# Kernel tuning notes

Measured on AMD Instinct MI355X. Metric: run time of the kernel, lower is better.

The kernel has to match this reference:

```python
import jax, jax.numpy as jnp
import numpy as np
import math

B, T, D = 1, 2048, 2048
H, HD = 16, 128          # n_head, head_dim = D // H
L = 512                  # latent_dims
RD = 64                  # rope_dims
K = 32                   # top-k selected tokens per query
THETA = 10000.0


def rope_tables(rd, t_max):
    freqs = 1.0 / (THETA ** (jnp.arange(0, rd, 2, dtype=jnp.float32) / rd))
    t = jnp.arange(t_max, dtype=jnp.float32)
    ang = jnp.outer(t, freqs)                      # (T, rd/2)
    cos = jnp.concatenate([jnp.cos(ang), jnp.cos(ang)], axis=-1)  # (T, rd)
    sin = jnp.concatenate([jnp.sin(ang), jnp.sin(ang)], axis=-1)
    return cos, sin


def rotate_half(x):
    d = x.shape[-1] // 2
    return jnp.concatenate([-x[..., d:], x[..., :d]], axis=-1)


def apply_rope(x, cos, sin):
    # x: (B, H, T, rd); cos/sin: (T, rd) -> broadcast over B, H
    t = x.shape[2]
    return x * cos[None, None, :t] + rotate_half(x) * sin[None, None, :t]


def setup_inputs() -> dict:
    key = jax.random.key(0)
    ks = jax.random.split(key, 10)
    s = lambda fan_in: 1.0 / math.sqrt(fan_in)
    inp = {
        'x': jax.random.normal(ks[0], (B, T, D), dtype=jnp.float32),
        'Wqd': jax.random.normal(ks[1], (D, L), dtype=jnp.float32) * s(D),
        'Wqu': jax.random.normal(ks[2], (L, D), dtype=jnp.float32) * s(L),
        'Wqr': jax.random.normal(ks[3], (L, H * RD), dtype=jnp.float32) * s(L),
        'Wkvd': jax.random.normal(ks[4], (D, L), dtype=jnp.float32) * s(D),
        'Wku': jax.random.normal(ks[5], (L, D), dtype=jnp.float32) * s(L),
        'Wvu': jax.random.normal(ks[6], (L, D), dtype=jnp.float32) * s(L),
        'Wkr': jax.random.normal(ks[7], (D, RD), dtype=jnp.float32) * s(D),
        'Wo': jax.random.normal(ks[8], (D, D), dtype=jnp.float32) * s(D),
        'topk_idx': jax.random.randint(ks[9], (B, T, K), 0, T, dtype=jnp.int64)
            if jax.config.jax_enable_x64 else
            jax.random.randint(ks[9], (B, T, K), 0, T, dtype=jnp.int32),
    }
    return inp


def reference(x, Wqd, Wqu, Wqr, Wkvd, Wku, Wvu, Wkr, Wo, topk_idx):
    cos, sin = rope_tables(RD, T)

    ql = x @ Wqd                                               # (B,T,L)
    q = (ql @ Wqu).reshape(B, T, H, HD).transpose(0, 2, 1, 3)  # (B,H,T,hd)
    qr = (ql @ Wqr).reshape(B, T, H, RD).transpose(0, 2, 1, 3)
    qr = apply_rope(qr, cos, sin)                              # (B,H,T,rd)

    ckv = x @ Wkvd                                             # (B,T,L)
    k = (ckv @ Wku).reshape(B, T, H, HD).transpose(0, 2, 1, 3) # (B,H,T,hd)
    v = (ckv @ Wvu).reshape(B, T, H, HD).transpose(0, 2, 1, 3)
    kr = apply_rope((x @ Wkr)[:, None], cos, sin)[:, 0]        # (B,T,rd) shared across heads

    # top-k gather sparse attention path
    flat = topk_idx.reshape(B, T * K)                          # (B, T*K)
    k_sel = jax.vmap(lambda a, i: a[:, i])(k, flat).reshape(B, H, T, K, HD)
    v_sel = jax.vmap(lambda a, i: a[:, i])(v, flat).reshape(B, H, T, K, HD)
    kr_sel = jax.vmap(lambda a, i: a[i])(kr, flat).reshape(B, T, K, RD)

    scale = 1.0 / math.sqrt(HD + RD)
    scores = (jnp.einsum('bhtd,bhtkd->bhtk', q, k_sel)
              + jnp.einsum('bhtd,btkd->bhtk', qr, kr_sel)) * scale
    attn = jax.nn.softmax(scores, axis=-1)                     # (B,H,T,K)
    out = jnp.einsum('bhtk,bhtkd->bhtd', attn, v_sel)          # (B,H,T,hd)
    out = out.transpose(0, 2, 1, 3).reshape(B, T, D)
    return out @ Wo
```

## Files before the change

### kernel.cpp

```cpp
#include <hip/hip_runtime.h>
#include <hip/hip_bf16.h>
#include <math.h>

typedef __hip_bfloat16 bf16;
typedef __attribute__((ext_vector_type(4))) float f32x4;
typedef __attribute__((ext_vector_type(8))) short s16x8;

#define T_SEQ 2048
#define DIM   2048
#define NH    16
#define LAT   512
#define RD    64
#define TOPK  32

typedef const __attribute__((address_space(1))) void* gas_ptr;
typedef __attribute__((address_space(3))) void* las_ptr;

struct GGroup {
    const bf16* A; const bf16* BT; bf16* C;
    int K, lda, ldb, ldc;
    int tx, ty, nz;
    long aZ, bZ, cZ;
    int tiles;
    int flags, N, t0;
};
struct GPack { GGroup g[4]; int n; };

template<int MT>
__global__ __launch_bounds__(256)
void gemm_group64(GPack gp)
{
    constexpr int MI = MT / 64;
    int b = blockIdx.x;
    int gi = 0;
    while (gi < gp.n - 1 && b >= gp.g[gi].tiles) { b -= gp.g[gi].tiles; ++gi; }
    const GGroup g = gp.g[gi];

    const int per_z = g.tx * g.ty;
    const int z   = b / per_z;
    const int rem = b - z * per_z;
    const int bx  = rem % g.tx;
    const int by  = rem / g.tx;

    const bf16* A  = g.A  + (size_t)z * g.aZ;
    const bf16* BT = g.BT + (size_t)z * g.bZ;
    bf16*       C  = g.C  + (size_t)z * g.cZ;

    __shared__ bf16 aL[MT * 64];
    __shared__ bf16 bL[64 * 64];

    const int tid  = threadIdx.x;
    const int wave = tid >> 6;
    const int lane = tid & 63;
    const int quad = lane >> 4;
    const int l16  = lane & 15;

    const int tile_m = by * MT;
    const int tile_n = bx * 64;
    const int wrow = wave * (MT / 4);

    const int lrow = lane >> 3;
    const int lke  = (((lane & 7) ^ lrow) * 8);
    const int sw   = l16 & 7;

    f32x4 acc[MI][4] = {};

    for (int k0 = 0; k0 < g.K; k0 += 64) {
#pragma unroll
        for (int p = 0; p < 2 * MI; ++p) {
            const int R = (wave * 2 * MI + p) * 8;
            const bf16* src = A + (size_t)(tile_m + R + lrow) * g.lda + k0 + lke;
            __builtin_amdgcn_global_load_lds((gas_ptr)src, (las_ptr)(aL + R * 64), 16, 0, 0);
        }
#pragma unroll
        for (int p = 0; p < 2; ++p) {
            const int R = (wave * 2 + p) * 8;
            const bf16* src = BT + (size_t)(tile_n + R + lrow) * g.ldb + k0 + lke;
            __builtin_amdgcn_global_load_lds((gas_ptr)src, (las_ptr)(bL + R * 64), 16, 0, 0);
        }
        __syncthreads();

#pragma unroll
        for (int ks = 0; ks < 2; ++ks) {
            s16x8 af[MI], bfr[4];
#pragma unroll
            for (int i = 0; i < MI; ++i)
                af[i] = *(const s16x8*)(&aL[(wrow + i * 16 + l16) * 64 +
                                            (((ks * 4 + quad) ^ sw) * 8)]);
#pragma unroll
            for (int j = 0; j < 4; ++j)
                bfr[j] = *(const s16x8*)(&bL[(j * 16 + l16) * 64 +
                                             (((ks * 4 + quad) ^ sw) * 8)]);

#pragma unroll
            for (int i = 0; i < MI; ++i)
#pragma unroll
                for (int j = 0; j < 4; ++j)
                    acc[i][j] = __builtin_amdgcn_mfma_f32_16x16x32_bf16(
                        af[i], bfr[j], acc[i][j], 0, 0, 0);
        }
        __syncthreads();
    }

    if (g.flags & 1) {
#pragma unroll
        for (int jp = 0; jp < 2; ++jp) {
            const int colL = tile_n + jp * 16 + l16;
            if ((g.flags & 2) && colL >= g.N) continue;
            const float fr = powf(10000.f, -(float)(jp * 16 + l16) / 32.f);
#pragma unroll
            for (int i = 0; i < MI; ++i) {
#pragma unroll
                for (int r = 0; r < 4; ++r) {
                    const int row = tile_m + wrow + i * 16 + quad * 4 + r;
                    float sv, cv;
                    sincosf((float)(g.t0 + row) * fr, &sv, &cv);
                    const float x0 = acc[i][jp][r];
                    const float x1 = acc[i][jp + 2][r];
                    C[(size_t)row * g.ldc + colL]      = __float2bfloat16(x0 * cv - x1 * sv);
                    C[(size_t)row * g.ldc + colL + 32] = __float2bfloat16(x1 * cv + x0 * sv);
                }
            }
        }
    } else if (g.flags & 4) {
        float* Cf = (float*)C;
#pragma unroll
        for (int j = 0; j < 4; ++j) {
            const int col = tile_n + j * 16 + l16;
#pragma unroll
            for (int i = 0; i < MI; ++i)
#pragma unroll
                for (int r = 0; r < 4; ++r) {
                    const int row = tile_m + wrow + i * 16 + quad * 4 + r;
                    Cf[(size_t)row * g.ldc + col] = acc[i][j][r];
                }
        }
    } else {
#pragma unroll
        for (int j = 0; j < 4; ++j) {
            const int col = tile_n + j * 16 + l16;
            if ((g.flags & 2) && col >= g.N) continue;
#pragma unroll
            for (int i = 0; i < MI; ++i)
#pragma unroll
                for (int r = 0; r < 4; ++r) {
                    const int row = tile_m + wrow + i * 16 + quad * 4 + r;
                    C[(size_t)row * g.ldc + col] = __float2bfloat16(acc[i][j][r]);
                }
        }
    }
}

struct TDesc { const float* src; bf16* dst; int R; int C; int tiles; int ctiles; };
struct TPack { TDesc d[8]; int n; };

__global__ __launch_bounds__(256)
void transpose_batch(TPack p)
{
    int b = blockIdx.x;
    int mi = 0;
    while (mi < p.n - 1 && b >= p.d[mi].tiles) { b -= p.d[mi].tiles; ++mi; }
    const TDesc d = p.d[mi];
    const int tr = b / d.ctiles, tc = b % d.ctiles;
    const int r0 = tr * 32, c0 = tc * 32;

    __shared__ float lds[32][33];
    const int tx = threadIdx.x & 31, ty = threadIdx.x >> 5;
#pragma unroll
    for (int i = 0; i < 4; ++i)
        lds[ty * 4 + i][tx] = d.src[(size_t)(r0 + ty * 4 + i) * d.C + c0 + tx];
    __syncthreads();
#pragma unroll
    for (int i = 0; i < 4; ++i)
        d.dst[(size_t)(c0 + ty * 4 + i) * d.R + r0 + tx] =
            __float2bfloat16(lds[tx][ty * 4 + i]);
}

__global__ __launch_bounds__(256)
void convert2(const float* s0, bf16* d0, int n0,
              const float* s1, bf16* d1, int n1)
{
    int i = blockIdx.x * blockDim.x + threadIdx.x;
    const float* s; bf16* d;
    if (i < n0) { s = s0; d = d0; }
    else if (i < n0 + n1) { i -= n0; s = s1; d = d1; }
    else return;
    const float4 a = *(const float4*)(s + (size_t)i * 8);
    const float4 b = *(const float4*)(s + (size_t)i * 8 + 4);
    bf16 t[8];
    t[0] = __float2bfloat16(a.x); t[1] = __float2bfloat16(a.y);
    t[2] = __float2bfloat16(a.z); t[3] = __float2bfloat16(a.w);
    t[4] = __float2bfloat16(b.x); t[5] = __float2bfloat16(b.y);
    t[6] = __float2bfloat16(b.z); t[7] = __float2bfloat16(b.w);
    *(uint4*)(d + (size_t)i * 8) = *(uint4*)t;
}

__global__ __launch_bounds__(256)
void attn_mla(const bf16* __restrict__ qt,
              const bf16* __restrict__ qr,
              const bf16* __restrict__ xw,
              const bf16* __restrict__ kr,
              const int*  __restrict__ topk,
              bf16* __restrict__ U,
              int t0)
{
    __shared__ short ckv_s[32 * 520];
    __shared__ short qt_s[16 * 520];
    __shared__ short kr_s[32 * 72];
    __shared__ short qr_s[16 * 72];
    __shared__ short P_s[4][16 * 40];
    __shared__ int   idx_s[32];

    const int tl   = blockIdx.x;
    const int tg   = t0 + tl;
    const int tid  = threadIdx.x;
    const int wv   = tid >> 6;
    const int lane = tid & 63;
    const int quad = lane >> 4;
    const int l16  = lane & 15;

    if (tid < 32) {
        int j = topk[(size_t)tg * TOPK + tid];
        idx_s[tid] = (j < 0 || j >= T_SEQ) ? 0 : j;
    }
    __syncthreads();

#pragma unroll
    for (int i = 0; i < 8; ++i) {
        const int row = wv * 8 + i;
        const int j = idx_s[row];
        __builtin_amdgcn_global_load_lds(
            (gas_ptr)(xw + (size_t)j * 1024 + 512 + lane * 8),
            (las_ptr)(ckv_s + row * 520), 16, 0, 0);
    }
#pragma unroll
    for (int i = 0; i < 4; ++i) {
        const int seg = wv * 4 + i;
        __builtin_amdgcn_global_load_lds(
            (gas_ptr)(qt + (size_t)tl * 8192 + seg * 512 + lane * 8),
            (las_ptr)(qt_s + seg * 520), 16, 0, 0);
    }
    {
        const int row = tid >> 3, seg = tid & 7;
        const int j = idx_s[row];
        *(uint4*)(kr_s + row * 72 + seg * 8) =
            *(const uint4*)(kr + (size_t)j * RD + seg * 8);
    }
    if (tid < 128) {
        const int head = tid >> 3, seg = tid & 7;
        *(uint4*)(qr_s + head * 72 + seg * 8) =
            *(const uint4*)(qr + (size_t)tl * 1024 + head * 64 + seg * 8);
    }
    __syncthreads();

    f32x4 sc[2] = {};
#pragma unroll
    for (int ks = 0; ks < 16; ++ks) {
        s16x8 a  = *(const s16x8*)(qt_s + l16 * 520 + ks * 32 + quad * 8);
        s16x8 b0 = *(const s16x8*)(ckv_s + l16 * 520 + ks * 32 + quad * 8);
        s16x8 b1 = *(const s16x8*)(ckv_s + (16 + l16) * 520 + ks * 32 + quad * 8);
        sc[0] = __builtin_amdgcn_mfma_f32_16x16x32_bf16(a, b0, sc[0], 0, 0, 0);
        sc[1] = __builtin_amdgcn_mfma_f32_16x16x32_bf16(a, b1, sc[1], 0, 0, 0);
    }
#pragma unroll
    for (int ks = 0; ks < 2; ++ks) {
        s16x8 a  = *(const s16x8*)(qr_s + l16 * 72 + ks * 32 + quad * 8);
        s16x8 b0 = *(const s16x8*)(kr_s + l16 * 72 + ks * 32 + quad * 8);
        s16x8 b1 = *(const s16x8*)(kr_s + (16 + l16) * 72 + ks * 32 + quad * 8);
        sc[0] = __builtin_amdgcn_mfma_f32_16x16x32_bf16(a, b0, sc[0], 0, 0, 0);
        sc[1] = __builtin_amdgcn_mfma_f32_16x16x32_bf16(a, b1, sc[1], 0, 0, 0);
    }

    const float scale = 0.0721687836487032f;
    float inv[4];
    short* pw = P_s[wv];
#pragma unroll
    for (int r = 0; r < 4; ++r) {
        float s0 = sc[0][r] * scale, s1 = sc[1][r] * scale;
        float mx = fmaxf(s0, s1);
#pragma unroll
        for (int off = 1; off < 16; off <<= 1) mx = fmaxf(mx, __shfl_xor(mx, off));
        float p0 = __expf(s0 - mx), p1 = __expf(s1 - mx);
        float l = p0 + p1;
#pragma unroll
        for (int off = 1; off < 16; off <<= 1) l += __shfl_xor(l, off);
        inv[r] = 1.f / l;
        pw[(quad * 4 + r) * 40 + l16]      = __builtin_bit_cast(short, __float2bfloat16(p0));
        pw[(quad * 4 + r) * 40 + 16 + l16] = __builtin_bit_cast(short, __float2bfloat16(p1));
    }

    s16x8 ap = *(const s16x8*)(pw + l16 * 40 + quad * 8);
#pragma unroll
    for (int tt = 0; tt < 8; ++tt) {
        const int n0 = wv * 128 + tt * 16;
        s16x8 b;
#pragma unroll
        for (int j = 0; j < 8; ++j)
            b[j] = ckv_s[(quad * 8 + j) * 520 + n0 + l16];
        f32x4 u = {};
        u = __builtin_amdgcn_mfma_f32_16x16x32_bf16(ap, b, u, 0, 0, 0);
#pragma unroll
        for (int r = 0; r < 4; ++r)
            U[(size_t)tl * 8192 + (quad * 4 + r) * 512 + n0 + l16] =
                __float2bfloat16(u[r] * inv[r]);
    }
}

extern "C" void kernel_launch(void* const* d_in, const int* in_sizes, int n_in,
                              void* d_out, int out_size, void* d_ws, size_t ws_size,
                              hipStream_t stream)
{
    const float* x    = (const float*)d_in[0];
    const float* Wqd  = (const float*)d_in[1];
    const float* Wqu  = (const float*)d_in[2];
    const float* Wqr  = (const float*)d_in[3];
    const float* Wkvd = (const float*)d_in[4];
    const float* Wku  = (const float*)d_in[5];
    const float* Wvu  = (const float*)d_in[6];
    const float* Wkr  = (const float*)d_in[7];
    const float* Wo   = (const float*)d_in[8];
    const int*   topk = (const int*)d_in[9];
    float* out = (float*)d_out;

    const size_t KB = 1024;
    char* ws = (char*)d_ws;
    const bool flat = ws_size >= (size_t)128000 * KB;
    const int  TCH  = flat ? 2048 : 512;
    const int  NCH  = T_SEQ / TCH;

    size_t oXB, oWxT, oWkrT, oWquT, oWkub, oWqrT, oWvuT, oQ, oXW, oKR,
           oQR, oO, oWoT, oQT, oU;
    if (flat) {
        oXB = 0;       oWxT = 8192;   oWkrT = 12288; oWquT = 12544;
        oWkub = 14592; oWqrT = 16640; oWvuT = 17664; oQ = 19712;
        oXW = 27904;   oKR = 32000;   oQR = 32256;   oO = 36352;
        oWoT = 44544;  oQT = 52736;   oU = 85504;
    } else {
        oXW = 0;       oKR = 4096;    oWquT = 4352;  oWkub = 6400;
        oWqrT = 8448;  oWvuT = 9472;  oO = 11520;    oXB = 19712;
        oWxT = 27904;  oWkrT = 32000; oQ = 19712;    oQT = 21760;
        oQR = 29952;   oU = 30976;    oWoT = 21760;
    }
    bf16* xb   = (bf16*)(ws + oXB * KB);
    bf16* WxT  = (bf16*)(ws + oWxT * KB);
    bf16* WkrT = (bf16*)(ws + oWkrT * KB);
    bf16* WquT = (bf16*)(ws + oWquT * KB);
    bf16* Wkub = (bf16*)(ws + oWkub * KB);
    bf16* WqrT = (bf16*)(ws + oWqrT * KB);
    bf16* WvuT = (bf16*)(ws + oWvuT * KB);
    bf16* qB   = (bf16*)(ws + oQ * KB);
    bf16* xw   = (bf16*)(ws + oXW * KB);
    bf16* kr   = (bf16*)(ws + oKR * KB);
    bf16* qrC  = (bf16*)(ws + oQR * KB);
    bf16* o    = (bf16*)(ws + oO * KB);
    bf16* WoT  = (bf16*)(ws + oWoT * KB);
    bf16* qtC  = (bf16*)(ws + oQT * KB);
    bf16* uC   = (bf16*)(ws + oU * KB);

    dim3 blk(256);

    {
        int n0 = T_SEQ * DIM / 8, n1 = LAT * DIM / 8;
        convert2<<<(n0 + n1 + 255) / 256, blk, 0, stream>>>(x, xb, n0, Wku, Wkub, n1);
        TPack p;
        p.d[0] = { Wqd,  WxT,                   DIM, LAT,  (DIM/32)*(LAT/32),  LAT/32 };
        p.d[1] = { Wkvd, WxT + (size_t)LAT*DIM, DIM, LAT,  (DIM/32)*(LAT/32),  LAT/32 };
        p.d[2] = { Wkr,  WkrT,                  DIM, RD,   (DIM/32)*(RD/32),   RD/32  };
        p.d[3] = { Wqr,  WqrT,                  LAT, 1024, (LAT/32)*(1024/32), 1024/32 };
        p.d[4] = { Wvu,  WvuT,                  LAT, DIM,  (LAT/32)*(DIM/32),  DIM/32 };
        p.d[5] = { Wqu,  WquT,                  LAT, DIM,  (LAT/32)*(DIM/32),  DIM/32 };
        p.n = 6;
        int tot = 0;
        for (int i = 0; i < p.n; ++i) tot += p.d[i].tiles;
        if (flat) {
            p.d[6] = { Wo, WoT, DIM, DIM, (DIM/32)*(DIM/32), DIM/32 };
            p.n = 7; tot += p.d[6].tiles;
        }
        transpose_batch<<<tot, blk, 0, stream>>>(p);
    }

    {
        GPack gp;
        gp.g[0] = { xb, WxT,  xw, DIM, DIM, DIM, 1024, 1024/64, T_SEQ/64, 1,
                    0, 0, 0, (1024/64)*(T_SEQ/64), 0, 1024, 0 };
        gp.g[1] = { xb, WkrT, kr, DIM, DIM, DIM, RD,   1,       T_SEQ/64, 1,
                    0, 0, 0, T_SEQ/64, 1 , RD, 0 };
        gp.n = 2;
        gemm_group64<64><<<gp.g[0].tiles + gp.g[1].tiles, blk, 0, stream>>>(gp);
    }

    for (int c = 0; c < NCH; ++c) {
        const int t0 = c * TCH;
        bf16* q  = flat ? qB  + (size_t)t0 * 2048 : qB;
        bf16* qt = flat ? qtC + (size_t)t0 * 8192 : qtC;
        bf16* qr = flat ? qrC + (size_t)t0 * 1024 : qrC;
        bf16* U  = flat ? uC  + (size_t)t0 * 8192 : uC;
        const bf16* xwc = xw + (size_t)t0 * 1024;

        {
            GPack gp;
            gp.g[0] = { xwc, WquT, q,  LAT, 1024, LAT, 2048, 2048/64, TCH/128, 1,
                        0, 0, 0, (2048/64)*(TCH/128), 0, 2048, 0 };
            gp.g[1] = { xwc, WqrT, qr, LAT, 1024, LAT, 1024, 1024/64, TCH/128, 1,
                        0, 0, 0, (1024/64)*(TCH/128), 1 , 1024, t0 };
            gp.n = 2;
            gemm_group64<128><<<gp.g[0].tiles + gp.g[1].tiles, blk, 0, stream>>>(gp);
        }
        {
            GPack gp;
            gp.g[0] = { q, Wkub, qt, 128, 2048, 2048, 8192, 512/64, TCH/128, NH,
                        128, 128, 512, (512/64)*(TCH/128)*NH, 0, 512, 0 };
            gp.n = 1;
            gemm_group64<128><<<gp.g[0].tiles, blk, 0, stream>>>(gp);
        }
        attn_mla<<<TCH, blk, 0, stream>>>(qt, qr, xw, kr, topk, U, t0);
        {
            GPack gp;
            gp.g[0] = { U, WvuT, o + (size_t)t0 * DIM, LAT, 8192, LAT, DIM,
                        2, TCH/128, NH, 512, (long)128*LAT, 128,
                        2*(TCH/128)*NH, 0, 128, 0 };
            gp.n = 1;
            gemm_group64<128><<<gp.g[0].tiles, blk, 0, stream>>>(gp);
        }
    }

    if (!flat) {
        TPack p;
        p.d[0] = { Wo, WoT, DIM, DIM, (DIM/32)*(DIM/32), DIM/32 };
        p.n = 1;
        transpose_batch<<<p.d[0].tiles, blk, 0, stream>>>(p);
    }
    {
        GPack gp;
        gp.g[0] = { o, WoT, (bf16*)out, DIM, DIM, DIM, DIM,
                    DIM/64, T_SEQ/128, 1, 0, 0, 0,
                    (DIM/64)*(T_SEQ/128), 4 , DIM, 0 };
        gp.n = 1;
        gemm_group64<128><<<gp.g[0].tiles, blk, 0, stream>>>(gp);
    }
}
```

Before: 248.4 us.

## Triple-buffer GEMM LDS tiles with async global-to-LDS prefetch pipeline

Converts the grouped GEMM main loop from a single LDS buffer with load-sync-compute-sync into a three-stage ring. Tiles are prefetched two iterations ahead via global_load_lds, and explicit vmcnt waits plus raw s_barrier replace __syncthreads. The goal is to hide global memory latency behind MFMA compute. In exchange it triples LDS use, which may lower occupancy, and relies on exact vmcnt accounting being correct.

```diff
diff --git a/kernel.cpp b/kernel.cpp
--- a/kernel.cpp
+++ b/kernel.cpp
@@ -28,9 +28,11 @@
 
 template<int MT>
 __global__ __launch_bounds__(256)
-void gemm_group64(GPack gp)
+void gemm_group(GPack gp)
 {
     constexpr int MI = MT / 64;
+    constexpr int L  = 2 * MI + 2;
+
     int b = blockIdx.x;
     int gi = 0;
     while (gi < gp.n - 1 && b >= gp.g[gi].tiles) { b -= gp.g[gi].tiles; ++gi; }
@@ -46,8 +48,8 @@
     const bf16* BT = g.BT + (size_t)z * g.bZ;
     bf16*       C  = g.C  + (size_t)z * g.cZ;
 
-    __shared__ bf16 aL[MT * 64];
-    __shared__ bf16 bL[64 * 64];
+    __shared__ bf16 aL[3][MT * 64];
+    __shared__ bf16 bL[3][64 * 64];
 
     const int tid  = threadIdx.x;
     const int wave = tid >> 6;
@@ -61,36 +63,56 @@
 
     const int lrow = lane >> 3;
     const int lke  = (((lane & 7) ^ lrow) * 8);
-    const int sw   = l16 & 7;
+    const int sw   = l16 & 15 & 7;
 
     f32x4 acc[MI][4] = {};
 
-    for (int k0 = 0; k0 < g.K; k0 += 64) {
+    const int nt = g.K >> 6;
+
+    auto stage = [&](int t, int sb) {
+        const int k0 = t << 6;
 #pragma unroll
         for (int p = 0; p < 2 * MI; ++p) {
             const int R = (wave * 2 * MI + p) * 8;
             const bf16* src = A + (size_t)(tile_m + R + lrow) * g.lda + k0 + lke;
-            __builtin_amdgcn_global_load_lds((gas_ptr)src, (las_ptr)(aL + R * 64), 16, 0, 0);
+            __builtin_amdgcn_global_load_lds((gas_ptr)src, (las_ptr)(aL[sb] + R * 64), 16, 0, 0);
         }
 #pragma unroll
         for (int p = 0; p < 2; ++p) {
             const int R = (wave * 2 + p) * 8;
             const bf16* src = BT + (size_t)(tile_n + R + lrow) * g.ldb + k0 + lke;
-            __builtin_amdgcn_global_load_lds((gas_ptr)src, (las_ptr)(bL + R * 64), 16, 0, 0);
-        }
-        __syncthreads();
+            __builtin_amdgcn_global_load_lds((gas_ptr)src, (las_ptr)(bL[sb] + R * 64), 16, 0, 0);
+        }
+    };
+
+    stage(0, 0);
+    if (nt > 1) stage(1, 1);
+
+    int s = 0;
+    for (int t = 0; t < nt; ++t) {
+        if (t + 2 < nt) {
+            int sn = s + 2; if (sn >= 3) sn -= 3;
+            stage(t + 2, sn);
+            asm volatile("s_waitcnt vmcnt(%0)" :: "n"(2 * L) : "memory");
+        } else if (t + 1 < nt) {
+            asm volatile("s_waitcnt vmcnt(%0)" :: "n"(L) : "memory");
+        } else {
+            asm volatile("s_waitcnt vmcnt(0)" ::: "memory");
+        }
+        __builtin_amdgcn_s_barrier();
+        asm volatile("" ::: "memory");
 
 #pragma unroll
         for (int ks = 0; ks < 2; ++ks) {
             s16x8 af[MI], bfr[4];
 #pragma unroll
             for (int i = 0; i < MI; ++i)
-                af[i] = *(const s16x8*)(&aL[(wrow + i * 16 + l16) * 64 +
-                                            (((ks * 4 + quad) ^ sw) * 8)]);
+                af[i] = *(const s16x8*)(&aL[s][(wrow + i * 16 + l16) * 64 +
+                                               (((ks * 4 + quad) ^ sw) * 8)]);
 #pragma unroll
             for (int j = 0; j < 4; ++j)
-                bfr[j] = *(const s16x8*)(&bL[(j * 16 + l16) * 64 +
-                                             (((ks * 4 + quad) ^ sw) * 8)]);
+                bfr[j] = *(const s16x8*)(&bL[s][(j * 16 + l16) * 64 +
+                                                (((ks * 4 + quad) ^ sw) * 8)]);
 
 #pragma unroll
             for (int i = 0; i < MI; ++i)
@@ -99,7 +121,9 @@
                     acc[i][j] = __builtin_amdgcn_mfma_f32_16x16x32_bf16(
                         af[i], bfr[j], acc[i][j], 0, 0, 0);
         }
-        __syncthreads();
+        asm volatile("" ::: "memory");
+        __builtin_amdgcn_s_barrier();
+        ++s; if (s >= 3) s = 0;
     }
 
     if (g.flags & 1) {
@@ -386,7 +410,7 @@
         gp.g[1] = { xb, WkrT, kr, DIM, DIM, DIM, RD,   1,       T_SEQ/64, 1,
                     0, 0, 0, T_SEQ/64, 1 , RD, 0 };
         gp.n = 2;
-        gemm_group64<64><<<gp.g[0].tiles + gp.g[1].tiles, blk, 0, stream>>>(gp);
+        gemm_group<64><<<gp.g[0].tiles + gp.g[1].tiles, blk, 0, stream>>>(gp);
     }
 
     for (int c = 0; c < NCH; ++c) {
@@ -404,14 +428,14 @@
             gp.g[1] = { xwc, WqrT, qr, LAT, 1024, LAT, 1024, 1024/64, TCH/128, 1,
                         0, 0, 0, (1024/64)*(TCH/128), 1 , 1024, t0 };
             gp.n = 2;
-            gemm_group64<128><<<gp.g[0].tiles + gp.g[1].tiles, blk, 0, stream>>>(gp);
+            gemm_group<128><<<gp.g[0].tiles + gp.g[1].tiles, blk, 0, stream>>>(gp);
         }
         {
             GPack gp;
             gp.g[0] = { q, Wkub, qt, 128, 2048, 2048, 8192, 512/64, TCH/128, NH,
                         128, 128, 512, (512/64)*(TCH/128)*NH, 0, 512, 0 };
             gp.n = 1;
-            gemm_group64<128><<<gp.g[0].tiles, blk, 0, stream>>>(gp);
+            gemm_group<128><<<gp.g[0].tiles, blk, 0, stream>>>(gp);
         }
         attn_mla<<<TCH, blk, 0, stream>>>(qt, qr, xw, kr, topk, U, t0);
         {
@@ -420,7 +444,7 @@
                         2, TCH/128, NH, 512, (long)128*LAT, 128,
                         2*(TCH/128)*NH, 0, 128, 0 };
             gp.n = 1;
-            gemm_group64<128><<<gp.g[0].tiles, blk, 0, stream>>>(gp);
+            gemm_group<128><<<gp.g[0].tiles, blk, 0, stream>>>(gp);
         }
     }
 
@@ -436,6 +460,6 @@
                     DIM/64, T_SEQ/128, 1, 0, 0, 0,
                     (DIM/64)*(T_SEQ/128), 4 , DIM, 0 };
         gp.n = 1;
-        gemm_group64<128><<<gp.g[0].tiles, blk, 0, stream>>>(gp);
+        gemm_group<128><<<gp.g[0].tiles, blk, 0, stream>>>(gp);
     }
 }
```

Result: no change. 250.8 us (+1.0%).
